# Performance work log

Measured on AMD Instinct MI355X. Metric: run time of the kernel, lower is better.

## Reference

```python
import jax, jax.numpy as jnp
import numpy as np


def setup_inputs() -> dict:
    key = jax.random.key(0)
    ks = jax.random.split(key, 8)
    B, C, L = 8, 512, 2048
    Cr = C // 8
    s = 1.0 / np.sqrt(C)
    return {
        "x": jax.random.normal(ks[0], (B, C, L), dtype=jnp.float32),
        "wq": jax.random.normal(ks[1], (Cr, C), dtype=jnp.float32) * s,
        "bq": jnp.zeros((Cr,), dtype=jnp.float32),
        "wk": jax.random.normal(ks[2], (Cr, C), dtype=jnp.float32) * s,
        "bk": jnp.zeros((Cr,), dtype=jnp.float32),
        "wv": jax.random.normal(ks[3], (C, C), dtype=jnp.float32) * s,
        "bv": jnp.zeros((C,), dtype=jnp.float32),
        "gamma": jnp.zeros((1,), dtype=jnp.float32),
    }


def reference(x, wq, bq, wk, bk, wv, bv, gamma):
    # 1x1 conv == pointwise linear over channels: [B,C,L] -> [B,Cout,L]
    q = jnp.einsum('oc,bcl->bol', wq, x) + bq[None, :, None]   # [B,C/8,L]
    k = jnp.einsum('oc,bcl->bol', wk, x) + bk[None, :, None]   # [B,C/8,L]
    v = jnp.einsum('oc,bcl->bol', wv, x) + bv[None, :, None]   # [B,C,L]
    # energy[b,i,j] = sum_d q[b,d,i] * k[b,d,j]  (no 1/sqrt(d) scaling, per source)
    energy = jnp.einsum('bdi,bdj->bij', q, k)                  # [B,L,L]
    attn = jax.nn.softmax(energy, axis=-1)                     # softmax over j
    # out[b,c,i] = sum_j v[b,c,j] * attn[b,i,j]
    out = jnp.einsum('bcj,bij->bci', v, attn)                  # [B,C,L]
    return gamma[0] * out + x
```

## Files before the change

### kernel.cpp

```cpp
#include <hip/hip_runtime.h>
#include <cmath>

#define LL  2048
#define CIN 512
#define CR  64
#define LOG2E 1.44269504088896340736f
#define M0   48.0f

typedef __bf16 bf16x8 __attribute__((ext_vector_type(8)));
typedef float f32x4 __attribute__((ext_vector_type(4)));
typedef unsigned int u32;
typedef unsigned short u16;
typedef unsigned long long u64;

__device__ __forceinline__ u16 f2bf(float f) {
  return __builtin_bit_cast(u16, (__bf16)f);
}
__device__ __forceinline__ bf16x8 ld8(const u16* p) {
  return *reinterpret_cast<const bf16x8*>(p);
}
__device__ __forceinline__ f32x4 mfma16(bf16x8 a, bf16x8 b, f32x4 c) {
  return __builtin_amdgcn_mfma_f32_16x16x32_bf16(a, b, c, 0, 0, 0);
}
__device__ __forceinline__ float fexp2(float x) {
#if __has_builtin(__builtin_amdgcn_exp2f)
  return __builtin_amdgcn_exp2f(x);
#else
  return exp2f(x);
#endif
}
__device__ __forceinline__ void barrier_lds_only() {
  asm volatile("s_waitcnt lgkmcnt(0)" ::: "memory");
  __builtin_amdgcn_s_barrier();
  asm volatile("" ::: "memory");
}
__device__ __forceinline__ u16* pp(u16* base, int row, int col) {
  u32 off = ((u32)row << 8) + ((u32)col << 1);
  off ^= ((u32)(row & 7) << 4);
  return (u16*)((char*)base + off);
}
__device__ __forceinline__ const u16* ppc(const u16* base, int row, int col) {
  u32 off = ((u32)row << 8) + ((u32)col << 1);
  off ^= ((u32)(row & 7) << 4);
  return (const u16*)((const char*)base + off);
}


__global__ void cvt_weights(const float* __restrict__ wq, const float* __restrict__ wk,
                            const float* __restrict__ wv, u16* __restrict__ out) {
  int i = blockIdx.x * 256 + threadIdx.x;
  float val; int rel; u16* dst;
  if (i < CR * CIN)          { rel = i;                val = wq[rel] * LOG2E; dst = out; }
  else if (i < 2 * CR * CIN) { rel = i - CR * CIN;     val = wk[rel];         dst = out + CR * CIN; }
  else                       { rel = i - 2 * CR * CIN; val = wv[rel];         dst = out + 2 * CR * CIN; }
  const int o = rel >> 9, c = rel & 511;
  dst[(size_t)((o >> 4) * 16 + (c >> 5)) * 512 + ((c & 31) >> 3) * 128 + (o & 15) * 8 + (c & 7)] = f2bf(val);
}

__global__ __launch_bounds__(256) void xpose(const float* __restrict__ X, u16* __restrict__ xF) {
  __shared__ u16 tile[64 * 72];
  const int bb = blockIdx.z;
  const int c0 = blockIdx.y * 64;
  const int i0 = blockIdx.x * 64;
  const int t  = threadIdx.x;
  const float* Xb = X + (size_t)bb * CIN * LL;
  u32* tile32 = (u32*)tile;
#pragma unroll
  for (int r = 0; r < 8; r++) {
    int idx = t + r * 256;
    int cw = idx >> 6, i = idx & 63;
    float f0 = Xb[(size_t)(c0 + 2 * cw) * LL + i0 + i];
    float f1 = Xb[(size_t)(c0 + 2 * cw + 1) * LL + i0 + i];
    tile32[i * 36 + cw] = (u32)f2bf(f0) | ((u32)f2bf(f1) << 16);
  }
  __syncthreads();
  const int w = t >> 6, l = t & 63;
  u16* out = xF + (size_t)bb * LL * CIN;
  const int igrp0 = i0 >> 4, cg0 = c0 >> 5;
#pragma unroll
  for (int q = 0; q < 2; q++) {
    const int f  = w * 2 + q;
    const int fi = f >> 1, fc = f & 1;
    bf16x8 vv = ld8(&tile[(fi * 16 + (l & 15)) * 72 + fc * 32 + (l >> 4) * 8]);
    *(bf16x8*)(out + (size_t)((igrp0 + fi) * 16 + cg0 + fc) * 512 + l * 8) = vv;
  }
}

__global__ __launch_bounds__(256, 4) void proj_all(
    const u16* __restrict__ xF, const u16* __restrict__ wqF, const u16* __restrict__ wkF,
    const u16* __restrict__ wvF, const float* __restrict__ bq, const float* __restrict__ bk,
    const float* __restrict__ bv,
    u16* __restrict__ qT, u16* __restrict__ kF, u16* __restrict__ vF)
{
  const int bb = blockIdx.z;
  const int bx = blockIdx.x;
  const int t  = threadIdx.x;
  const int w  = t >> 6, l = t & 63;
  const int li = l & 15, g = l >> 4;
  const u16* xFb = xF + (size_t)bb * LL * CIN;

  if (bx < 64) {
    const int i0 = bx * 32;
    const int igrp0 = bx * 2;
    const int proj = w >> 1;
    const int oh = (w & 1) * 32;
    const int rg0 = oh >> 4;
    const u16* Wf = proj ? wkF : wqF;
    const float* Bs = proj ? bk : bq;
    const float bscale = proj ? 1.0f : LOG2E;

    f32x4 acc[2][2];
#pragma unroll
    for (int mt = 0; mt < 2; mt++)
#pragma unroll
      for (int nt = 0; nt < 2; nt++) acc[mt][nt] = f32x4{0.f, 0.f, 0.f, 0.f};

    bf16x8 aA[2], bA[2], aB[2], bB[2];
#define LDQK(af, bf2, cg)                                                  \
    do {                                                                   \
      af[0]  = ld8(xFb + (size_t)((igrp0    ) * 16 + (cg)) * 512 + l * 8); \
      af[1]  = ld8(xFb + (size_t)((igrp0 + 1) * 16 + (cg)) * 512 + l * 8); \
      bf2[0] = ld8(Wf  + (size_t)((rg0      ) * 16 + (cg)) * 512 + l * 8); \
      bf2[1] = ld8(Wf  + (size_t)((rg0   + 1) * 16 + (cg)) * 512 + l * 8); \
    } while (0)

    LDQK(aA, bA, 0);
#pragma unroll
    for (int cg = 0; cg < 16; cg += 2) {
      LDQK(aB, bB, cg + 1);
#pragma unroll
      for (int mt = 0; mt < 2; mt++)
#pragma unroll
        for (int nt = 0; nt < 2; nt++) acc[mt][nt] = mfma16(aA[mt], bA[nt], acc[mt][nt]);
      if (cg + 2 < 16) LDQK(aA, bA, cg + 2);
#pragma unroll
      for (int mt = 0; mt < 2; mt++)
#pragma unroll
        for (int nt = 0; nt < 2; nt++) acc[mt][nt] = mfma16(aB[mt], bB[nt], acc[mt][nt]);
    }
#undef LDQK

    if (proj == 0) {
      u16* Out = qT + (size_t)bb * LL * CR;
#pragma unroll
      for (int mt = 0; mt < 2; mt++)
#pragma unroll
        for (int nt = 0; nt < 2; nt++) {
          const int o = oh + nt * 16 + li;
          const float bias = Bs[o] * bscale;
#pragma unroll
          for (int r = 0; r < 4; r++) {
            const int i = i0 + mt * 16 + g * 4 + r;
            Out[(size_t)i * CR + o] = f2bf(acc[mt][nt][r] + bias);
          }
        }
    } else {
      u16* Out = kF + (size_t)bb * LL * CR;
      const int kk = oh >> 5;
#pragma unroll
      for (int mt = 0; mt < 2; mt++) {
        const int jgrp = (i0 >> 4) + mt;
#pragma unroll
        for (int nt = 0; nt < 2; nt++) {
          const int o = oh + nt * 16 + li;
          const float bias = Bs[o] * bscale;
          const int shi = (nt * 2 + (li >> 3)) * 16;
          const int e   = li & 7;
#pragma unroll
          for (int r = 0; r < 4; r++) {
            const int slot = shi + g * 4 + r;
            Out[(size_t)(jgrp * 2 + kk) * 512 + slot * 8 + e] = f2bf(acc[mt][nt][r] + bias);
          }
        }
      }
    }
  } else {
    const int vx = bx - 64;
    const int i0 = (vx & 31) * 64;
    const int o0 = (vx >> 5) * 64;
    const int igrp_v = (i0 >> 4) + w;
    const int rgv0 = o0 >> 4;

    f32x4 acc[4];
#pragma unroll
    for (int mt = 0; mt < 4; mt++) acc[mt] = f32x4{0.f, 0.f, 0.f, 0.f};

    bf16x8 xA, aA[4], xB, aB[4];
#define LDV(xf, af, cg)                                                      \
    do {                                                                     \
      xf    = ld8(xFb + (size_t)(igrp_v * 16 + (cg)) * 512 + l * 8);         \
      af[0] = ld8(wvF + (size_t)((rgv0    ) * 16 + (cg)) * 512 + l * 8);     \
      af[1] = ld8(wvF + (size_t)((rgv0 + 1) * 16 + (cg)) * 512 + l * 8);     \
      af[2] = ld8(wvF + (size_t)((rgv0 + 2) * 16 + (cg)) * 512 + l * 8);     \
      af[3] = ld8(wvF + (size_t)((rgv0 + 3) * 16 + (cg)) * 512 + l * 8);     \
    } while (0)

    LDV(xA, aA, 0);
#pragma unroll
    for (int cg = 0; cg < 16; cg += 2) {
      LDV(xB, aB, cg + 1);
#pragma unroll
      for (int mt = 0; mt < 4; mt++) acc[mt] = mfma16(aA[mt], xA, acc[mt]);
      if (cg + 2 < 16) LDV(xA, aA, cg + 2);
#pragma unroll
      for (int mt = 0; mt < 4; mt++) acc[mt] = mfma16(aB[mt], xB, acc[mt]);
    }
#undef LDV

    u16* Vb = vF + (size_t)bb * CIN * LL;
    const int jg2 = (i0 >> 5) + (w >> 1);
    const int gg  = (w & 1) * 2 + (li >> 3);
    const int e   = li & 7;
#pragma unroll
    for (int mt = 0; mt < 4; mt++) {
      const int cgrp = (o0 >> 4) + mt;
#pragma unroll
      for (int r = 0; r < 4; r++) {
        const int o = o0 + mt * 16 + g * 4 + r;
        const int slot = gg * 16 + (g * 4 + r);
        Vb[(size_t)(cgrp * 64 + jg2) * 512 + slot * 8 + e] = f2bf(acc[mt][r] + bv[o]);
      }
    }
  }
}

__global__ __launch_bounds__(512, 2) void attn_mfma(
    const u16* __restrict__ qT, const u16* __restrict__ kF, const u16* __restrict__ vF,
    const float* __restrict__ X, const float* __restrict__ Gamma, float* __restrict__ Y,
    int nb)
{
  __shared__ u16 Pls[2][64 * 128];
  __shared__ float lsb[8][64];
  const int bid  = blockIdx.x;
  const int bb   = bid % nb;
  const int i0   = (bid / nb) * 64;
  const int t    = threadIdx.x;
  const int w    = t >> 6, l = t & 63;
  const int li   = l & 15, g = l >> 4;
  const int c0   = w * 64;
  const int cg0  = c0 >> 4;
  const u16* qTb = qT + (size_t)bb * LL * CR;
  const u16* kFb = kF + (size_t)bb * LL * CR;
  const u16* vFb = vF + (size_t)bb * CIN * LL;

  bf16x8 qf[4][2];
#pragma unroll
  for (int ni = 0; ni < 4; ni++)
#pragma unroll
    for (int kk = 0; kk < 2; kk++)
      qf[ni][kk] = ld8(qTb + (size_t)(i0 + ni * 16 + li) * CR + kk * 32 + g * 8);

  f32x4 acc[4][4];
#pragma unroll
  for (int mC = 0; mC < 4; mC++)
#pragma unroll
    for (int ni = 0; ni < 4; ni++) acc[mC][ni] = f32x4{0.f, 0.f, 0.f, 0.f};
  float lsum[4] = {0.f, 0.f, 0.f, 0.f};

  bf16x8 kfc[2], kfn[2];
  kfc[0] = ld8(kFb + (size_t)(w * 2 + 0) * 512 + l * 8);
  kfc[1] = ld8(kFb + (size_t)(w * 2 + 1) * 512 + l * 8);
  bf16x8 vA[4], vB[4], vC[4], vD[4];
#pragma unroll
  for (int mC = 0; mC < 4; mC++)
    vA[mC] = ld8(vFb + (size_t)((cg0 + mC) * 64 + 0) * 512 + l * 8);
#pragma unroll
  for (int mC = 0; mC < 4; mC++)
    vB[mC] = ld8(vFb + (size_t)((cg0 + mC) * 64 + 1) * 512 + l * 8);

#pragma unroll 1
  for (int jt = 0; jt < LL; jt += 128) {
    u16* Pbuf = Pls[(jt >> 7) & 1];
    const int jn  = (jt + 128 < LL) ? jt + 128 : 0;
    const int jg  = jt >> 5;
    const int jgn = jn >> 5;

    f32x4 s[4];
#pragma unroll
    for (int ni = 0; ni < 4; ni++) {
      s[ni] = mfma16(kfc[0], qf[ni][0], f32x4{0.f, 0.f, 0.f, 0.f});
      s[ni] = mfma16(kfc[1], qf[ni][1], s[ni]);
    }
    kfn[0] = ld8(kFb + (size_t)((((jn >> 4) + w) * 2 + 0)) * 512 + l * 8);
    kfn[1] = ld8(kFb + (size_t)((((jn >> 4) + w) * 2 + 1)) * 512 + l * 8);
#pragma unroll
    for (int mC = 0; mC < 4; mC++)
      vC[mC] = ld8(vFb + (size_t)((cg0 + mC) * 64 + jg + 2) * 512 + l * 8);
#pragma unroll
    for (int mC = 0; mC < 4; mC++)
      vD[mC] = ld8(vFb + (size_t)((cg0 + mC) * 64 + jg + 3) * 512 + l * 8);
    __builtin_amdgcn_sched_barrier(0);

    const int colb = w * 16 + g * 4;
#pragma unroll
    for (int ni = 0; ni < 4; ni++) {
      const float e0 = fexp2(s[ni][0] - M0);
      const float e1 = fexp2(s[ni][1] - M0);
      const float e2 = fexp2(s[ni][2] - M0);
      const float e3 = fexp2(s[ni][3] - M0);
      lsum[ni] += (e0 + e1) + (e2 + e3);
      u32 lo = (u32)f2bf(e0) | ((u32)f2bf(e1) << 16);
      u32 hi = (u32)f2bf(e2) | ((u32)f2bf(e3) << 16);
      *(u64*)pp(Pbuf, ni * 16 + li, colb) = ((u64)hi << 32) | lo;
    }

    barrier_lds_only();

    bf16x8 pf[4];
#pragma unroll
    for (int ni = 0; ni < 4; ni++) pf[ni] = ld8(ppc(Pbuf, ni * 16 + li, 0 * 32 + g * 8));
    __builtin_amdgcn_s_setprio(1);
#pragma unroll
    for (int mC = 0; mC < 4; mC++)
#pragma unroll
      for (int ni = 0; ni < 4; ni++) acc[mC][ni] = mfma16(vA[mC], pf[ni], acc[mC][ni]);
    __builtin_amdgcn_s_setprio(0);
#pragma unroll
    for (int mC = 0; mC < 4; mC++)
      vA[mC] = ld8(vFb + (size_t)((cg0 + mC) * 64 + jgn + 0) * 512 + l * 8);
    __builtin_amdgcn_sched_barrier(0);
#pragma unroll
    for (int ni = 0; ni < 4; ni++) pf[ni] = ld8(ppc(Pbuf, ni * 16 + li, 1 * 32 + g * 8));
    __builtin_amdgcn_s_setprio(1);
#pragma unroll
    for (int mC = 0; mC < 4; mC++)
#pragma unroll
      for (int ni = 0; ni < 4; ni++) acc[mC][ni] = mfma16(vB[mC], pf[ni], acc[mC][ni]);
    __builtin_amdgcn_s_setprio(0);
#pragma unroll
    for (int mC = 0; mC < 4; mC++)
      vB[mC] = ld8(vFb + (size_t)((cg0 + mC) * 64 + jgn + 1) * 512 + l * 8);
    __builtin_amdgcn_sched_barrier(0);
#pragma unroll
    for (int ni = 0; ni < 4; ni++) pf[ni] = ld8(ppc(Pbuf, ni * 16 + li, 2 * 32 + g * 8));
    __builtin_amdgcn_s_setprio(1);
#pragma unroll
    for (int mC = 0; mC < 4; mC++)
#pragma unroll
      for (int ni = 0; ni < 4; ni++) acc[mC][ni] = mfma16(vC[mC], pf[ni], acc[mC][ni]);
    __builtin_amdgcn_s_setprio(0);
#pragma unroll
    for (int ni = 0; ni < 4; ni++) pf[ni] = ld8(ppc(Pbuf, ni * 16 + li, 3 * 32 + g * 8));
    __builtin_amdgcn_s_setprio(1);
#pragma unroll
    for (int mC = 0; mC < 4; mC++)
#pragma unroll
      for (int ni = 0; ni < 4; ni++) acc[mC][ni] = mfma16(vD[mC], pf[ni], acc[mC][ni]);
    __builtin_amdgcn_s_setprio(0);

    kfc[0] = kfn[0];
    kfc[1] = kfn[1];
  }

#pragma unroll
  for (int ni = 0; ni < 4; ni++) {
    lsum[ni] += __shfl_xor(lsum[ni], 16);
    lsum[ni] += __shfl_xor(lsum[ni], 32);
  }
  if (g == 0) {
#pragma unroll
    for (int ni = 0; ni < 4; ni++) lsb[w][ni * 16 + li] = lsum[ni];
  }
  __syncthreads();
  float linv[4];
#pragma unroll
  for (int ni = 0; ni < 4; ni++) {
    const int i = ni * 16 + li;
    float s8 = lsb[0][i] + lsb[1][i] + lsb[2][i] + lsb[3][i]
             + lsb[4][i] + lsb[5][i] + lsb[6][i] + lsb[7][i];
    linv[ni] = 1.0f / s8;
  }

  const float gamma = Gamma[0];
  const float* Xb = X + (size_t)bb * CIN * LL;
  float*       Yb = Y + (size_t)bb * CIN * LL;
#pragma unroll
  for (int mC = 0; mC < 4; mC++)
#pragma unroll
    for (int ni = 0; ni < 4; ni++)
#pragma unroll
      for (int r = 0; r < 4; r++) {
        const int c = c0 + mC * 16 + g * 4 + r;
        const int i = i0 + ni * 16 + li;
        const size_t off = (size_t)c * LL + i;
        Yb[off] = gamma * acc[mC][ni][r] * linv[ni] + Xb[off];
      }
}

extern "C" void kernel_launch(void* const* d_in, const int* in_sizes, int n_in,
                              void* d_out, int out_size, void* d_ws, size_t ws_size,
                              hipStream_t stream) {
  const float* x  = (const float*)d_in[0];
  const float* wq = (const float*)d_in[1];
  const float* bq = (const float*)d_in[2];
  const float* wk = (const float*)d_in[3];
  const float* bk = (const float*)d_in[4];
  const float* wv = (const float*)d_in[5];
  const float* bv = (const float*)d_in[6];
  const float* gm = (const float*)d_in[7];
  float* y = (float*)d_out;

  u16* wqF = (u16*)d_ws;
  u16* wkF = wqF + (size_t)CR * CIN;
  u16* wvF = wkF + (size_t)CR * CIN;
  u16* dyn = wvF + (size_t)CIN * CIN;
  const size_t wbytes = ((size_t)2 * CR * CIN + (size_t)CIN * CIN) * 2;
  const size_t perb = ((size_t)LL * CIN + 2 * (size_t)LL * CR + (size_t)CIN * LL);
  int nbc = 8;
  while (nbc > 1 && ws_size < wbytes + perb * 2 * (size_t)nbc) nbc >>= 1;

  const dim3 blk(256, 1, 1);
  const int nw = 2 * CR * CIN + CIN * CIN;
  hipLaunchKernelGGL(cvt_weights, dim3((nw + 255) / 256), blk, 0, stream, wq, wk, wv, wqF);

  for (int b0 = 0; b0 < 8; b0 += nbc) {
    const int nb = (8 - b0 < nbc) ? (8 - b0) : nbc;
    u16* xF = dyn;
    u16* qT = xF + (size_t)nb * LL * CIN;
    u16* kF = qT + (size_t)nb * LL * CR;
    u16* vF = kF + (size_t)nb * LL * CR;
    const float* xb = x + (size_t)b0 * CIN * LL;
    float*       yb = y + (size_t)b0 * CIN * LL;

    hipLaunchKernelGGL(xpose, dim3(LL / 64, CIN / 64, nb), blk, 0, stream, xb, xF);
    hipLaunchKernelGGL(proj_all, dim3(320, 1, nb), blk, 0, stream,
                       xF, wqF, wkF, wvF, bq, bk, bv, qT, kF, vF);
    hipLaunchKernelGGL(attn_mfma, dim3(32 * nb, 1, 1), dim3(512, 1, 1), 0, stream,
                       qT, kF, vF, xb, gm, yb, nb);
  }
}
```

Baseline: 92.29 us.

## Split attention blocks over channel quarters with 4-wave blocks and simpler loop

The attention kernel now launches four times as many 256-thread blocks. Each block handles a 64-query tile and 128 output channels instead of all 512, which raises parallelism and occupancy. The cost is that QK^T and the exponentials are recomputed four times, once per channel quarter. The software-pipelined register prefetch of K and V tiles, along with the sched_barriers, is replaced by straightforward loads inside the loop.

```diff
diff --git a/kernel.cpp b/kernel.cpp
--- a/kernel.cpp
+++ b/kernel.cpp
@@ -224,21 +224,22 @@
   }
 }
 
-__global__ __launch_bounds__(512, 2) void attn_mfma(
+__global__ __launch_bounds__(256, 3) void attn_mfma(
     const u16* __restrict__ qT, const u16* __restrict__ kF, const u16* __restrict__ vF,
     const float* __restrict__ X, const float* __restrict__ Gamma, float* __restrict__ Y,
     int nb)
 {
   __shared__ u16 Pls[2][64 * 128];
-  __shared__ float lsb[8][64];
+  __shared__ float lsb[4][64];
   const int bid  = blockIdx.x;
   const int bb   = bid % nb;
-  const int i0   = (bid / nb) * 64;
+  const int rest = bid / nb;
+  const int i0   = (rest >> 2) * 64;
+  const int ch   = (rest & 3) * 128;
   const int t    = threadIdx.x;
   const int w    = t >> 6, l = t & 63;
   const int li   = l & 15, g = l >> 4;
-  const int c0   = w * 64;
-  const int cg0  = c0 >> 4;
+  const int cg0  = (ch + w * 32) >> 4;
   const u16* qTb = qT + (size_t)bb * LL * CR;
   const u16* kFb = kF + (size_t)bb * LL * CR;
   const u16* vFb = vF + (size_t)bb * CIN * LL;
@@ -250,106 +251,66 @@
     for (int kk = 0; kk < 2; kk++)
       qf[ni][kk] = ld8(qTb + (size_t)(i0 + ni * 16 + li) * CR + kk * 32 + g * 8);
 
-  f32x4 acc[4][4];
-#pragma unroll
-  for (int mC = 0; mC < 4; mC++)
+  f32x4 acc[2][4];
+#pragma unroll
+  for (int mC = 0; mC < 2; mC++)
 #pragma unroll
     for (int ni = 0; ni < 4; ni++) acc[mC][ni] = f32x4{0.f, 0.f, 0.f, 0.f};
   float lsum[4] = {0.f, 0.f, 0.f, 0.f};
-
-  bf16x8 kfc[2], kfn[2];
-  kfc[0] = ld8(kFb + (size_t)(w * 2 + 0) * 512 + l * 8);
-  kfc[1] = ld8(kFb + (size_t)(w * 2 + 1) * 512 + l * 8);
-  bf16x8 vA[4], vB[4], vC[4], vD[4];
-#pragma unroll
-  for (int mC = 0; mC < 4; mC++)
-    vA[mC] = ld8(vFb + (size_t)((cg0 + mC) * 64 + 0) * 512 + l * 8);
-#pragma unroll
-  for (int mC = 0; mC < 4; mC++)
-    vB[mC] = ld8(vFb + (size_t)((cg0 + mC) * 64 + 1) * 512 + l * 8);
 
 #pragma unroll 1
   for (int jt = 0; jt < LL; jt += 128) {
     u16* Pbuf = Pls[(jt >> 7) & 1];
-    const int jn  = (jt + 128 < LL) ? jt + 128 : 0;
-    const int jg  = jt >> 5;
-    const int jgn = jn >> 5;
-
-    f32x4 s[4];
-#pragma unroll
-    for (int ni = 0; ni < 4; ni++) {
-      s[ni] = mfma16(kfc[0], qf[ni][0], f32x4{0.f, 0.f, 0.f, 0.f});
-      s[ni] = mfma16(kfc[1], qf[ni][1], s[ni]);
-    }
-    kfn[0] = ld8(kFb + (size_t)((((jn >> 4) + w) * 2 + 0)) * 512 + l * 8);
-    kfn[1] = ld8(kFb + (size_t)((((jn >> 4) + w) * 2 + 1)) * 512 + l * 8);
-#pragma unroll
-    for (int mC = 0; mC < 4; mC++)
-      vC[mC] = ld8(vFb + (size_t)((cg0 + mC) * 64 + jg + 2) * 512 + l * 8);
-#pragma unroll
-    for (int mC = 0; mC < 4; mC++)
-      vD[mC] = ld8(vFb + (size_t)((cg0 + mC) * 64 + jg + 3) * 512 + l * 8);
-    __builtin_amdgcn_sched_barrier(0);
-
-    const int colb = w * 16 + g * 4;
-#pragma unroll
-    for (int ni = 0; ni < 4; ni++) {
-      const float e0 = fexp2(s[ni][0] - M0);
-      const float e1 = fexp2(s[ni][1] - M0);
-      const float e2 = fexp2(s[ni][2] - M0);
-      const float e3 = fexp2(s[ni][3] - M0);
-      lsum[ni] += (e0 + e1) + (e2 + e3);
-      u32 lo = (u32)f2bf(e0) | ((u32)f2bf(e1) << 16);
-      u32 hi = (u32)f2bf(e2) | ((u32)f2bf(e3) << 16);
-      *(u64*)pp(Pbuf, ni * 16 + li, colb) = ((u64)hi << 32) | lo;
+    const int jw = jt + w * 32;
+
+    bf16x8 kf[2][2];
+#pragma unroll
+    for (int mt = 0; mt < 2; mt++)
+#pragma unroll
+      for (int kk = 0; kk < 2; kk++)
+        kf[mt][kk] = ld8(kFb + (size_t)((((jw >> 4) + mt) * 2 + kk)) * 512 + l * 8);
+#pragma unroll
+    for (int mt = 0; mt < 2; mt++) {
+      f32x4 s[4];
+#pragma unroll
+      for (int ni = 0; ni < 4; ni++) {
+        s[ni] = mfma16(kf[mt][0], qf[ni][0], f32x4{0.f, 0.f, 0.f, 0.f});
+        s[ni] = mfma16(kf[mt][1], qf[ni][1], s[ni]);
+      }
+      const int colb = w * 32 + mt * 16 + g * 4;
+#pragma unroll
+      for (int ni = 0; ni < 4; ni++) {
+        const float e0 = fexp2(s[ni][0] - M0);
+        const float e1 = fexp2(s[ni][1] - M0);
+        const float e2 = fexp2(s[ni][2] - M0);
+        const float e3 = fexp2(s[ni][3] - M0);
+        lsum[ni] += (e0 + e1) + (e2 + e3);
+        u32 lo = (u32)f2bf(e0) | ((u32)f2bf(e1) << 16);
+        u32 hi = (u32)f2bf(e2) | ((u32)f2bf(e3) << 16);
+        *(u64*)pp(Pbuf, ni * 16 + li, colb) = ((u64)hi << 32) | lo;
+      }
     }
 
     barrier_lds_only();
 
-    bf16x8 pf[4];
-#pragma unroll
-    for (int ni = 0; ni < 4; ni++) pf[ni] = ld8(ppc(Pbuf, ni * 16 + li, 0 * 32 + g * 8));
-    __builtin_amdgcn_s_setprio(1);
-#pragma unroll
-    for (int mC = 0; mC < 4; mC++)
-#pragma unroll
-      for (int ni = 0; ni < 4; ni++) acc[mC][ni] = mfma16(vA[mC], pf[ni], acc[mC][ni]);
-    __builtin_amdgcn_s_setprio(0);
-#pragma unroll
-    for (int mC = 0; mC < 4; mC++)
-      vA[mC] = ld8(vFb + (size_t)((cg0 + mC) * 64 + jgn + 0) * 512 + l * 8);
-    __builtin_amdgcn_sched_barrier(0);
-#pragma unroll
-    for (int ni = 0; ni < 4; ni++) pf[ni] = ld8(ppc(Pbuf, ni * 16 + li, 1 * 32 + g * 8));
-    __builtin_amdgcn_s_setprio(1);
-#pragma unroll
-    for (int mC = 0; mC < 4; mC++)
-#pragma unroll
-      for (int ni = 0; ni < 4; ni++) acc[mC][ni] = mfma16(vB[mC], pf[ni], acc[mC][ni]);
-    __builtin_amdgcn_s_setprio(0);
-#pragma unroll
-    for (int mC = 0; mC < 4; mC++)
-      vB[mC] = ld8(vFb + (size_t)((cg0 + mC) * 64 + jgn + 1) * 512 + l * 8);
-    __builtin_amdgcn_sched_barrier(0);
-#pragma unroll
-    for (int ni = 0; ni < 4; ni++) pf[ni] = ld8(ppc(Pbuf, ni * 16 + li, 2 * 32 + g * 8));
-    __builtin_amdgcn_s_setprio(1);
-#pragma unroll
-    for (int mC = 0; mC < 4; mC++)
-#pragma unroll
-      for (int ni = 0; ni < 4; ni++) acc[mC][ni] = mfma16(vC[mC], pf[ni], acc[mC][ni]);
-    __builtin_amdgcn_s_setprio(0);
-#pragma unroll
-    for (int ni = 0; ni < 4; ni++) pf[ni] = ld8(ppc(Pbuf, ni * 16 + li, 3 * 32 + g * 8));
-    __builtin_amdgcn_s_setprio(1);
-#pragma unroll
-    for (int mC = 0; mC < 4; mC++)
-#pragma unroll
-      for (int ni = 0; ni < 4; ni++) acc[mC][ni] = mfma16(vD[mC], pf[ni], acc[mC][ni]);
-    __builtin_amdgcn_s_setprio(0);
-
-    kfc[0] = kfn[0];
-    kfc[1] = kfn[1];
+#pragma unroll
+    for (int ks = 0; ks < 4; ks++) {
+      bf16x8 vf[2];
+#pragma unroll
+      for (int mC = 0; mC < 2; mC++)
+        vf[mC] = ld8(vFb + (size_t)((cg0 + mC) * 64 + (jt >> 5) + ks) * 512 + l * 8);
+      bf16x8 pf[4];
+#pragma unroll
+      for (int ni = 0; ni < 4; ni++)
+        pf[ni] = ld8(ppc(Pbuf, ni * 16 + li, ks * 32 + g * 8));
+      __builtin_amdgcn_s_setprio(1);
+#pragma unroll
+      for (int mC = 0; mC < 2; mC++)
+#pragma unroll
+        for (int ni = 0; ni < 4; ni++)
+          acc[mC][ni] = mfma16(vf[mC], pf[ni], acc[mC][ni]);
+      __builtin_amdgcn_s_setprio(0);
+    }
   }
 
 #pragma unroll
@@ -362,29 +323,24 @@
     for (int ni = 0; ni < 4; ni++) lsb[w][ni * 16 + li] = lsum[ni];
   }
   __syncthreads();
-  float linv[4];
-#pragma unroll
-  for (int ni = 0; ni < 4; ni++) {
-    const int i = ni * 16 + li;
-    float s8 = lsb[0][i] + lsb[1][i] + lsb[2][i] + lsb[3][i]
-             + lsb[4][i] + lsb[5][i] + lsb[6][i] + lsb[7][i];
-    linv[ni] = 1.0f / s8;
-  }
 
   const float gamma = Gamma[0];
   const float* Xb = X + (size_t)bb * CIN * LL;
   float*       Yb = Y + (size_t)bb * CIN * LL;
 #pragma unroll
-  for (int mC = 0; mC < 4; mC++)
-#pragma unroll
-    for (int ni = 0; ni < 4; ni++)
+  for (int ni = 0; ni < 4; ni++) {
+    const int q = ni * 16 + li;
+    const float linv = 1.0f / (lsb[0][q] + lsb[1][q] + lsb[2][q] + lsb[3][q]);
+    const int i = i0 + q;
+#pragma unroll
+    for (int mC = 0; mC < 2; mC++)
 #pragma unroll
       for (int r = 0; r < 4; r++) {
-        const int c = c0 + mC * 16 + g * 4 + r;
-        const int i = i0 + ni * 16 + li;
+        const int c = ch + w * 32 + mC * 16 + g * 4 + r;
         const size_t off = (size_t)c * LL + i;
-        Yb[off] = gamma * acc[mC][ni][r] * linv[ni] + Xb[off];
-      }
+        Yb[off] = gamma * acc[mC][ni][r] * linv + Xb[off];
+      }
+  }
 }
 
 extern "C" void kernel_launch(void* const* d_in, const int* in_sizes, int n_in,
@@ -425,7 +381,7 @@
     hipLaunchKernelGGL(xpose, dim3(LL / 64, CIN / 64, nb), blk, 0, stream, xb, xF);
     hipLaunchKernelGGL(proj_all, dim3(320, 1, nb), blk, 0, stream,
                        xF, wqF, wkF, wvF, bq, bk, bv, qT, kF, vF);
-    hipLaunchKernelGGL(attn_mfma, dim3(32 * nb, 1, 1), dim3(512, 1, 1), 0, stream,
+    hipLaunchKernelGGL(attn_mfma, dim3(128 * nb, 1, 1), blk, 0, stream,
                        qT, kF, vF, xb, gm, yb, nb);
   }
 }
```

After: 130.2 us. +41.1%, slower.
